# Performance work log

Hardware: AMD Instinct MI355X
Metric: run time of the kernel (lower is better)

## Reference

```python
import jax, jax.numpy as jnp
import numpy as np

D = 64          # slot_size == in_features
S = 8           # num_slots
H = 128         # mlp_hidden_size
N_ITER = 3
EPS = 1e-8


def _ln(x, g, b, eps=1e-5):
    m = jnp.mean(x, axis=-1, keepdims=True)
    v = jnp.var(x, axis=-1, keepdims=True)
    return (x - m) * jax.lax.rsqrt(v + eps) * g + b


def _gru(x, h, w_ih, w_hh, b_ih, b_hh):
    # torch.nn.GRUCell semantics, gate order r, z, n
    gi = x @ w_ih.T + b_ih
    gh = h @ w_hh.T + b_hh
    i_r, i_z, i_n = jnp.split(gi, 3, axis=-1)
    h_r, h_z, h_n = jnp.split(gh, 3, axis=-1)
    r = jax.nn.sigmoid(i_r + h_r)
    z = jax.nn.sigmoid(i_z + h_z)
    n = jnp.tanh(i_n + r * h_n)
    return (1.0 - z) * n + z * h


def setup_inputs() -> dict:
    key = jax.random.key(0)
    ks = jax.random.split(key, 16)
    sc = 0.02
    inp = {
        'inputs': jax.random.normal(ks[0], (64, 16384, D), jnp.float32),
        'slots_init': jax.random.normal(ks[1], (64, S, D), jnp.float32),
        'ln_in_g': jnp.ones((D,), jnp.float32), 'ln_in_b': jnp.zeros((D,), jnp.float32),
        'ln_s_g': jnp.ones((D,), jnp.float32), 'ln_s_b': jnp.zeros((D,), jnp.float32),
        'ln_m_g': jnp.ones((D,), jnp.float32), 'ln_m_b': jnp.zeros((D,), jnp.float32),
        'Wq': jax.random.normal(ks[2], (D, D), jnp.float32) * sc,
        'Wk': jax.random.normal(ks[3], (D, D), jnp.float32) * sc,
        'Wv': jax.random.normal(ks[4], (D, D), jnp.float32) * sc,
        'w_ih': jax.random.normal(ks[5], (3 * D, D), jnp.float32) * sc,
        'w_hh': jax.random.normal(ks[6], (3 * D, D), jnp.float32) * sc,
        'b_ih': jnp.zeros((3 * D,), jnp.float32),
        'b_hh': jnp.zeros((3 * D,), jnp.float32),
        'W1': jax.random.normal(ks[7], (H, D), jnp.float32) * sc,
        'b1': jnp.zeros((H,), jnp.float32),
        'W2': jax.random.normal(ks[8], (D, H), jnp.float32) * sc,
        'b2': jnp.zeros((D,), jnp.float32),
        'slots_mu': jax.random.normal(ks[9], (1, 1, D), jnp.float32) * sc,
        'slots_log_sigma': jax.random.normal(ks[10], (1, 1, D), jnp.float32) * sc,
    }
    return inp


def reference(inputs, slots_init, ln_in_g, ln_in_b, ln_s_g, ln_s_b, ln_m_g, ln_m_b,
              Wq, Wk, Wv, w_ih, w_hh, b_ih, b_hh, W1, b1, W2, b2,
              slots_mu, slots_log_sigma):
    B, N, _ = inputs.shape
    x = _ln(inputs, ln_in_g, ln_in_b)
    k = x @ Wk.T                               # [B, N, D]
    v = x @ Wv.T                               # [B, N, D]
    slots = slots_mu + jnp.exp(slots_log_sigma) * slots_init  # [B, S, D]
    scale = D ** -0.5
    attns = None
    for it in range(N_ITER):
        slots_prev = slots
        sn = _ln(slots, ln_s_g, ln_s_b)
        q = sn @ Wq.T                          # [B, S, D]
        logits = scale * jnp.einsum('bnd,bsd->bns', k, q)  # [B, N, S]
        attn = jax.nn.softmax(logits, axis=-1)
        if it == 0:
            attns = jax.lax.stop_gradient(attn)  # clone().detach() on first iter
        else:
            attns = attns + attn
        a = attn + EPS
        a = a / jnp.sum(a, axis=1, keepdims=True)  # normalize over inputs
        updates = jnp.einsum('bns,bnd->bsd', a, v)  # [B, S, D]
        h = _gru(updates.reshape(B * S, D), slots_prev.reshape(B * S, D),
                 w_ih, w_hh, b_ih, b_hh).reshape(B, S, D)
        mlp_out = jnp.maximum(_ln(h, ln_m_g, ln_m_b) @ W1.T + b1, 0.0) @ W2.T + b2
        slots = h + mlp_out
    return slots, attns / N_ITER
```

## Files before the change

### kernel.cpp

```cpp
#include <hip/hip_runtime.h>
#include <math.h>

#define Dk 64
#define Sk 8
#define Nk 16384
#define Bk 64
#define Hk 128
#define BSD (Bk*Sk*Dk)

typedef __attribute__((ext_vector_type(8))) short   bf16x8;
typedef __attribute__((ext_vector_type(4))) float   f32x4;
typedef __attribute__((ext_vector_type(2))) unsigned int u32x2;
typedef __attribute__((ext_vector_type(4))) unsigned int u32x4;

union FragU { u32x4 u; bf16x8 s; };

__device__ __forceinline__ unsigned short f2b(float f){
  unsigned u = __float_as_uint(f);
  unsigned r = (u + 0x7FFFu + ((u>>16)&1u)) >> 16;
  return (unsigned short)r;
}
__device__ __forceinline__ unsigned pk2(float a, float b){
  return (unsigned)f2b(a) | ((unsigned)f2b(b)<<16);
}
__device__ __forceinline__ bf16x8 mkfrag(unsigned a0,unsigned a1,unsigned a2,unsigned a3){
  FragU x; x.u = (u32x4){a0,a1,a2,a3}; return x.s;
}
__device__ __forceinline__ bf16x8 mkfrag2(u32x2 a, u32x2 b){
  FragU x; x.u = (u32x4){a.x,a.y,b.x,b.y}; return x.s;
}
__device__ __forceinline__ float wsum64(float v){
  #pragma unroll
  for (int m=1;m<64;m<<=1) v += __shfl_xor(v,m,64);
  return v;
}
__device__ __forceinline__ f32x4 ntld4(const float* p){
  return __builtin_nontemporal_load((const f32x4*)p);
}

#define MFMA16(a,b,c) __builtin_amdgcn_mfma_f32_16x16x32_bf16(a,b,c,0,0,0)
#define TRRD(dst, addr)          asm volatile("ds_read_b64_tr_b16 %0, %1"              : "=v"(dst) : "v"(addr) : "memory")
#define TRRD_O(dst, addr, OFF)   asm volatile("ds_read_b64_tr_b16 %0, %1 offset:" #OFF : "=v"(dst) : "v"(addr) : "memory")

template<int MODE, int LAST>
__global__ __launch_bounds__(256,4) void iter_kernel(
    const float* __restrict__ inp, unsigned short* __restrict__ xbf,
    const float* __restrict__ ln_g, const float* __restrict__ ln_b,
    const float* __restrict__ qtb,
    float* __restrict__ attns_out,
    float* __restrict__ Upart,
    float* __restrict__ denpart)
{
  constexpr int NQ = LAST ? 3 : 1;
  __shared__ unsigned short shmem[4*2688];
  __shared__ float ured[4][512];
  __shared__ float dred[4][8];

  const int t   = threadIdx.x;
  const int wid = t>>6, l = t&63;
  const int r16 = l&15, g = l>>4;
  unsigned short* sh = &shmem[wid*2688];
  const unsigned ldsb = (unsigned)(unsigned long long)(void*)sh;

  const int blk = blockIdx.x;
  const int gw  = blk*4 + wid;
  const int b   = gw>>7;
  const int w0  = (gw&127)*4;

  bf16x8 qf0[NQ], qf1[NQ];
  #pragma unroll
  for (int it=0; it<NQ; ++it){
    const float* qp = qtb + (size_t)it*BSD + (size_t)((b<<3) + (r16&7))*Dk + g*8;
    f32x4 a0 = *(const f32x4*)(qp);    f32x4 a1 = *(const f32x4*)(qp+4);
    f32x4 c0 = *(const f32x4*)(qp+32); f32x4 c1 = *(const f32x4*)(qp+36);
    qf0[it] = mkfrag(pk2(a0.x,a0.y),pk2(a0.z,a0.w),pk2(a1.x,a1.y),pk2(a1.z,a1.w));
    qf1[it] = mkfrag(pk2(c0.x,c0.y),pk2(c0.z,c0.w),pk2(c1.x,c1.y),pk2(c1.z,c1.w));
  }

  f32x4 uacc0={0.f,0.f,0.f,0.f}, uacc1={0.f,0.f,0.f,0.f};
  f32x4 uacc2={0.f,0.f,0.f,0.f}, uacc3={0.f,0.f,0.f,0.f};
  f32x4 dacc = {0.f,0.f,0.f,0.f};

  f32x4 gv0,gv1,gv2,gv3, bv0,bv1,bv2,bv3;
  if (MODE==0){
    const float* gp  = ln_g + g*8;      const float* bp  = ln_b + g*8;
    const float* gp2 = ln_g + 32 + g*8; const float* bp2 = ln_b + 32 + g*8;
    gv0=*(const f32x4*)gp;  gv1=*(const f32x4*)(gp+4);
    gv2=*(const f32x4*)gp2; gv3=*(const f32x4*)(gp2+4);
    bv0=*(const f32x4*)bp;  bv1=*(const f32x4*)(bp+4);
    bv2=*(const f32x4*)bp2; bv3=*(const f32x4*)(bp2+4);
  }

  f32x4 nx[2][4];
  u32x4 np[2][2];
  u32x4 fr[2][2];

  auto LOADW = [&](int w){
    const size_t base = (size_t)b*Nk + (size_t)(w0+w)*32;
    #pragma unroll
    for (int rt=0; rt<2; ++rt){
      const size_t row = base + rt*16 + r16;
      if (MODE==0){
        const float* s0 = inp + row*Dk + g*8;
        const float* s1 = inp + row*Dk + 32 + g*8;
        nx[rt][0]=ntld4(s0); nx[rt][1]=ntld4(s0+4);
        nx[rt][2]=ntld4(s1); nx[rt][3]=ntld4(s1+4);
      } else {
        const unsigned short* sp = xbf + row*Dk;
        np[rt][0] = *(const u32x4*)(sp + g*8);
        np[rt][1] = *(const u32x4*)(sp + 32 + g*8);
      }
    }
  };

  auto PROCESS = [&](int w){
    const size_t base = (size_t)b*Nk + (size_t)(w0+w)*32;
    #pragma unroll
    for (int rt=0; rt<2; ++rt){
      const int rloc = rt*16 + r16;
      u32x4 q0, q1;
      if (MODE==0){
        f32x4 x0=nx[rt][0], x1=nx[rt][1], x2=nx[rt][2], x3=nx[rt][3];
        float s1 = (x0.x+x0.y+x0.z+x0.w)+(x1.x+x1.y+x1.z+x1.w)
                 + (x2.x+x2.y+x2.z+x2.w)+(x3.x+x3.y+x3.z+x3.w);
        float s2 = x0.x*x0.x+x0.y*x0.y+x0.z*x0.z+x0.w*x0.w
                 + x1.x*x1.x+x1.y*x1.y+x1.z*x1.z+x1.w*x1.w
                 + x2.x*x2.x+x2.y*x2.y+x2.z*x2.z+x2.w*x2.w
                 + x3.x*x3.x+x3.y*x3.y+x3.z*x3.z+x3.w*x3.w;
        s1 += __shfl_xor(s1,16,64); s1 += __shfl_xor(s1,32,64);
        s2 += __shfl_xor(s2,16,64); s2 += __shfl_xor(s2,32,64);
        const float mean = s1*(1.f/64.f);
        const float rstd = rsqrtf(s2*(1.f/64.f) - mean*mean + 1e-5f);
        x0 = (x0-mean)*rstd*gv0 + bv0;  x1 = (x1-mean)*rstd*gv1 + bv1;
        x2 = (x2-mean)*rstd*gv2 + bv2;  x3 = (x3-mean)*rstd*gv3 + bv3;
        q0 = (u32x4){pk2(x0.x,x0.y),pk2(x0.z,x0.w),pk2(x1.x,x1.y),pk2(x1.z,x1.w)};
        q1 = (u32x4){pk2(x2.x,x2.y),pk2(x2.z,x2.w),pk2(x3.x,x3.y),pk2(x3.z,x3.w)};
        const size_t row = base + rloc;
        *(u32x4*)(xbf + row*Dk + g*8)      = q0;
        *(u32x4*)(xbf + row*Dk + 32 + g*8) = q1;
      } else {
        q0 = np[rt][0]; q1 = np[rt][1];
      }
      fr[rt][0] = q0; fr[rt][1] = q1;
      const int i0 = (g>>1)*528     + rloc*16 + (g&1)*8;
      const int i1 = ((g>>1)+2)*528 + rloc*16 + (g&1)*8;
      *(u32x4*)&sh[i0] = q0;
      *(u32x4*)&sh[i1] = q1;
    }
  };

  LOADW(0); PROCESS(0); LOADW(1);

  for (int w4=0; w4<4; ++w4){
    const size_t rowwin = (size_t)b*Nk + (size_t)(w0+w4)*32;

    #pragma unroll
    for (int rt=0; rt<2; ++rt){
      FragU fl, fh; fl.u = fr[rt][0]; fh.u = fr[rt][1];
      const bf16x8 xl = fl.s, xh = fh.s;
      f32x4 asum = {0.f,0.f,0.f,0.f};
      f32x4 atc;
      #pragma unroll
      for (int it=0; it<NQ; ++it){
        f32x4 c = {0.f,0.f,0.f,0.f};
        c = MFMA16(qf0[it], xl, c);
        c = MFMA16(qf1[it], xh, c);
        float mx = fmaxf(fmaxf(c.x,c.y), fmaxf(c.z,c.w));
        mx = fmaxf(mx, __shfl_xor(mx,16,64));
        f32x4 e;
        e.x = __expf(c.x-mx); e.y = __expf(c.y-mx);
        e.z = __expf(c.z-mx); e.w = __expf(c.w-mx);
        float es = e.x+e.y+e.z+e.w;
        es += __shfl_xor(es,16,64);
        f32x4 at = e*(1.f/es);
        if (LAST) asum = asum + at;
        atc = at;
      }
      if (LAST && l < 32){
        f32x4 nv = asum*(1.f/3.f);
        __builtin_nontemporal_store(nv,
            (f32x4*)(attns_out + (rowwin + rt*16 + r16)*Sk + g*4));
      }
      f32x4 a = atc + 1e-8f;
      dacc = dacc + a;
      u32x2 pk = {pk2(a.x,a.y), pk2(a.z,a.w)};
      *(u32x2*)&sh[2112 + (rt*16+r16)*16 + g*4] = pk;
    }

    u32x2 p0,p1, b00,b01,b10,b11,b20,b21,b30,b31;
    const unsigned xA = ldsb + g*256 + r16*2;
    const unsigned pA = ldsb + 4224 + g*256 + r16*2;
    TRRD  (b00, xA);          TRRD_O(b01, xA, 128);
    TRRD_O(b10, xA, 1056);    TRRD_O(b11, xA, 1184);
    TRRD_O(b20, xA, 2112);    TRRD_O(b21, xA, 2240);
    TRRD_O(b30, xA, 3168);    TRRD_O(b31, xA, 3296);
    TRRD  (p0, pA);           TRRD_O(p1, pA, 128);

    if (w4 < 3) PROCESS(w4+1);
    if (w4 < 2) LOADW(w4+2);

    if (w4 < 3) asm volatile("s_waitcnt lgkmcnt(4)" ::: "memory");
    else        asm volatile("s_waitcnt lgkmcnt(0)" ::: "memory");
    __builtin_amdgcn_sched_barrier(0);

    const bf16x8 pf = mkfrag2(p0,p1);
    uacc0 = MFMA16(pf, mkfrag2(b00,b01), uacc0);
    uacc1 = MFMA16(pf, mkfrag2(b10,b11), uacc1);
    uacc2 = MFMA16(pf, mkfrag2(b20,b21), uacc2);
    uacc3 = MFMA16(pf, mkfrag2(b30,b31), uacc3);
  }

  float dd0=dacc.x, dd1=dacc.y, dd2=dacc.z, dd3=dacc.w;
  #pragma unroll
  for (int m=1;m<16;m<<=1){
    dd0 += __shfl_xor(dd0,m,64); dd1 += __shfl_xor(dd1,m,64);
    dd2 += __shfl_xor(dd2,m,64); dd3 += __shfl_xor(dd3,m,64);
  }
  if (l < 32){
    #pragma unroll
    for (int j=0;j<4;++j){
      ured[wid][(g*4+j)*64 +  0 + r16] = uacc0[j];
      ured[wid][(g*4+j)*64 + 16 + r16] = uacc1[j];
      ured[wid][(g*4+j)*64 + 32 + r16] = uacc2[j];
      ured[wid][(g*4+j)*64 + 48 + r16] = uacc3[j];
    }
    if (r16 == 0){
      dred[wid][g*4+0]=dd0; dred[wid][g*4+1]=dd1;
      dred[wid][g*4+2]=dd2; dred[wid][g*4+3]=dd3;
    }
  }
  __syncthreads();
  #pragma unroll
  for (int e=t; e<512; e+=256){
    Upart[(size_t)blk*512 + e] = ured[0][e]+ured[1][e]+ured[2][e]+ured[3][e];
  }
  if (t < 8) denpart[blk*8 + t] = dred[0][t]+dred[1][t]+dred[2][t]+dred[3][t];
}

__global__ __launch_bounds__(64) void slot_kernel(
    const float* __restrict__ slots_init,
    const float* __restrict__ mu, const float* __restrict__ lsig,
    const float* __restrict__ ln_s_g, const float* __restrict__ ln_s_b,
    const float* __restrict__ ln_m_g, const float* __restrict__ ln_m_b,
    const float* __restrict__ Wq, const float* __restrict__ Wk, const float* __restrict__ Wv,
    const float* __restrict__ w_ih, const float* __restrict__ w_hh,
    const float* __restrict__ b_ih, const float* __restrict__ b_hh,
    const float* __restrict__ W1, const float* __restrict__ b1,
    const float* __restrict__ W2, const float* __restrict__ b2,
    float* __restrict__ slots, const float* __restrict__ Upart,
    const float* __restrict__ denpart,
    float* __restrict__ qt_out, float* __restrict__ slots_out, int mode)
{
  __shared__ float sh[Hk];
  __shared__ float shh[Dk];
  const int d  = threadIdx.x;
  const int bs = blockIdx.x;

  float snew;
  if (mode == 0) {
    snew = mu[d] + expf(lsig[d]) * slots_init[bs*Dk + d];
  } else {
    const int b8 = bs>>3, s = bs&7;
    const float* up = Upart + (size_t)(b8*32)*512 + s*64 + d;
    float uval = 0.f;
    #pragma unroll 8
    for (int k2=0;k2<32;++k2) uval += up[k2*512];
    float dp = (d<32) ? denpart[(b8*32+d)*8 + s] : 0.f;
    const float dn = wsum64(dp);

    sh[d] = uval;
    __syncthreads();
    float num = 0.f;
    #pragma unroll
    for (int j=0;j<Dk;j+=4){
      float4 w = *(const float4*)&Wv[d*Dk+j];
      num += sh[j]*w.x + sh[j+1]*w.y + sh[j+2]*w.z + sh[j+3]*w.w;
    }
    const float upd = num / dn;
    const float h = slots[bs*Dk + d];
    __syncthreads();
    sh[d] = upd; shh[d] = h;
    __syncthreads();

    float gi_r=b_ih[d], gi_z=b_ih[Dk+d], gi_n=b_ih[2*Dk+d];
    float gh_r=b_hh[d], gh_z=b_hh[Dk+d], gh_n=b_hh[2*Dk+d];
    #pragma unroll 4
    for (int j=0;j<Dk;j+=4){
      const float x0=sh[j],  x1=sh[j+1],  x2=sh[j+2],  x3=sh[j+3];
      const float h0=shh[j], h1=shh[j+1], h2=shh[j+2], h3=shh[j+3];
      float4 w;
      w = *(const float4*)&w_ih[d*Dk+j];        gi_r += x0*w.x+x1*w.y+x2*w.z+x3*w.w;
      w = *(const float4*)&w_ih[(Dk+d)*Dk+j];   gi_z += x0*w.x+x1*w.y+x2*w.z+x3*w.w;
      w = *(const float4*)&w_ih[(2*Dk+d)*Dk+j]; gi_n += x0*w.x+x1*w.y+x2*w.z+x3*w.w;
      w = *(const float4*)&w_hh[d*Dk+j];        gh_r += h0*w.x+h1*w.y+h2*w.z+h3*w.w;
      w = *(const float4*)&w_hh[(Dk+d)*Dk+j];   gh_z += h0*w.x+h1*w.y+h2*w.z+h3*w.w;
      w = *(const float4*)&w_hh[(2*Dk+d)*Dk+j]; gh_n += h0*w.x+h1*w.y+h2*w.z+h3*w.w;
    }
    const float rg = 1.f/(1.f+expf(-(gi_r+gh_r)));
    const float zg = 1.f/(1.f+expf(-(gi_z+gh_z)));
    const float ng = tanhf(gi_n + rg*gh_n);
    const float hn = (1.f-zg)*ng + zg*h;

    const float m  = wsum64(hn)*(1.f/64.f);
    const float dv = hn - m;
    const float vr = wsum64(dv*dv)*(1.f/64.f);
    const float mv = dv*rsqrtf(vr+1e-5f)*ln_m_g[d] + ln_m_b[d];
    __syncthreads();
    sh[d] = mv;
    __syncthreads();

    float h1a = b1[d], h2a = b1[Dk+d];
    #pragma unroll 4
    for (int j=0;j<Dk;j+=4){
      const float x0=sh[j], x1=sh[j+1], x2=sh[j+2], x3=sh[j+3];
      float4 w;
      w = *(const float4*)&W1[d*Dk+j];      h1a += x0*w.x+x1*w.y+x2*w.z+x3*w.w;
      w = *(const float4*)&W1[(Dk+d)*Dk+j]; h2a += x0*w.x+x1*w.y+x2*w.z+x3*w.w;
    }
    h1a = fmaxf(h1a, 0.f); h2a = fmaxf(h2a, 0.f);
    __syncthreads();
    sh[d] = h1a; sh[Dk+d] = h2a;
    __syncthreads();
    float o = b2[d];
    #pragma unroll 4
    for (int tt=0;tt<Hk;tt+=4){
      float4 w = *(const float4*)&W2[d*Hk+tt];
      o += sh[tt]*w.x + sh[tt+1]*w.y + sh[tt+2]*w.z + sh[tt+3]*w.w;
    }
    snew = hn + o;
  }

  if (slots_out){ slots_out[bs*Dk + d] = snew; return; }
  slots[bs*Dk + d] = snew;

  const float m2  = wsum64(snew)*(1.f/64.f);
  const float dv2 = snew - m2;
  const float vr2 = wsum64(dv2*dv2)*(1.f/64.f);
  const float sn  = dv2*rsqrtf(vr2+1e-5f)*ln_s_g[d] + ln_s_b[d];
  __syncthreads();
  sh[d] = sn;
  __syncthreads();
  float q = 0.f;
  #pragma unroll
  for (int j=0;j<Dk;j+=4){
    float4 w = *(const float4*)&Wq[d*Dk+j];
    q += sh[j]*w.x + sh[j+1]*w.y + sh[j+2]*w.z + sh[j+3]*w.w;
  }
  __syncthreads();
  sh[d] = q;
  __syncthreads();
  float qt = 0.f;
  for (int dd=0; dd<Dk; ++dd) qt += sh[dd]*Wk[dd*Dk + d];
  qt_out[bs*Dk + d] = qt * 0.125f;
}

extern "C" void kernel_launch(void* const* d_in, const int* in_sizes, int n_in,
                              void* d_out, int out_size, void* d_ws, size_t ws_size,
                              hipStream_t stream)
{
  const float* inp     = (const float*)d_in[0];
  const float* sinit   = (const float*)d_in[1];
  const float* ln_in_g = (const float*)d_in[2];
  const float* ln_in_b = (const float*)d_in[3];
  const float* ln_s_g  = (const float*)d_in[4];
  const float* ln_s_b  = (const float*)d_in[5];
  const float* ln_m_g  = (const float*)d_in[6];
  const float* ln_m_b  = (const float*)d_in[7];
  const float* Wq      = (const float*)d_in[8];
  const float* Wk      = (const float*)d_in[9];
  const float* Wv      = (const float*)d_in[10];
  const float* w_ih    = (const float*)d_in[11];
  const float* w_hh    = (const float*)d_in[12];
  const float* b_ih    = (const float*)d_in[13];
  const float* b_hh    = (const float*)d_in[14];
  const float* W1      = (const float*)d_in[15];
  const float* b1      = (const float*)d_in[16];
  const float* W2      = (const float*)d_in[17];
  const float* b2      = (const float*)d_in[18];
  const float* mu      = (const float*)d_in[19];
  const float* lsig    = (const float*)d_in[20];

  float* out       = (float*)d_out;
  float* out_slots = out;
  float* out_attns = out + BSD;

  char* w = (char*)d_ws;
  float* slots   = (float*)(w);
  float* qtbuf   = (float*)(w + 131072);
  float* Upart   = (float*)(w + 655360);
  float* denpart = (float*)(w + 4849664);
  unsigned short* xbf = (unsigned short*)(w + 4915200);

  float* qt0 = qtbuf;
  float* qt1 = qtbuf + BSD;
  float* qt2 = qtbuf + 2*BSD;
  float* qt3 = qtbuf + 3*BSD;

  slot_kernel<<<Bk*Sk, Dk, 0, stream>>>(sinit, mu, lsig, ln_s_g, ln_s_b, ln_m_g, ln_m_b,
      Wq, Wk, Wv, w_ih, w_hh, b_ih, b_hh, W1, b1, W2, b2,
      slots, Upart, denpart, qt0, nullptr, 0);

  iter_kernel<0,0><<<2048, 256, 0, stream>>>(
      inp, xbf, ln_in_g, ln_in_b, qt0, out_attns, Upart, denpart);
  slot_kernel<<<Bk*Sk, Dk, 0, stream>>>(sinit, mu, lsig, ln_s_g, ln_s_b, ln_m_g, ln_m_b,
      Wq, Wk, Wv, w_ih, w_hh, b_ih, b_hh, W1, b1, W2, b2,
      slots, Upart, denpart, qt1, nullptr, 1);

  iter_kernel<1,0><<<2048, 256, 0, stream>>>(
      inp, xbf, ln_in_g, ln_in_b, qt1, out_attns, Upart, denpart);
  slot_kernel<<<Bk*Sk, Dk, 0, stream>>>(sinit, mu, lsig, ln_s_g, ln_s_b, ln_m_g, ln_m_b,
      Wq, Wk, Wv, w_ih, w_hh, b_ih, b_hh, W1, b1, W2, b2,
      slots, Upart, denpart, qt2, nullptr, 1);

  iter_kernel<1,1><<<2048, 256, 0, stream>>>(
      inp, xbf, ln_in_g, ln_in_b, qtbuf, out_attns, Upart, denpart);
  slot_kernel<<<Bk*Sk, Dk, 0, stream>>>(sinit, mu, lsig, ln_s_g, ln_s_b, ln_m_g, ln_m_b,
      Wq, Wk, Wv, w_ih, w_hh, b_ih, b_hh, W1, b1, W2, b2,
      slots, Upart, denpart, qt3, out_slots, 1);
}
```

Before: 232.1 us.

## Fuse slot GRU/MLP update into iteration kernels and halve grid size

Folds the per-slot GRU, MLP and query projection into the prologue of each attention iteration kernel. Every block recomputes the slot state for its batch redundantly from the previous iteration's partial sums, which removes three small slot_kernel launches and the serial gaps between kernels. The grid drops from 2048 to 1024 blocks, and each wave now processes 8 windows instead of 4, which halves the number of partials. The cost is redundant slot math in every block (16x per batch) and a longer prologue before streaming begins. Partial buffers are double-buffered per iteration to avoid read/write hazards.

```diff
diff --git a/kernel.cpp b/kernel.cpp
--- a/kernel.cpp
+++ b/kernel.cpp
@@ -41,20 +41,125 @@
 #define MFMA16(a,b,c) __builtin_amdgcn_mfma_f32_16x16x32_bf16(a,b,c,0,0,0)
 #define TRRD(dst, addr)          asm volatile("ds_read_b64_tr_b16 %0, %1"              : "=v"(dst) : "v"(addr) : "memory")
 #define TRRD_O(dst, addr, OFF)   asm volatile("ds_read_b64_tr_b16 %0, %1 offset:" #OFF : "=v"(dst) : "v"(addr) : "memory")
-
-template<int MODE, int LAST>
+#define LGKM0 asm volatile("s_waitcnt lgkmcnt(0)" ::: "memory")
+
+__device__ __forceinline__ float gru_mlp_step(
+    int d, float uval, float dn, float h,
+    const float* __restrict__ Wv,
+    const float* __restrict__ w_ih, const float* __restrict__ w_hh,
+    const float* __restrict__ b_ih, const float* __restrict__ b_hh,
+    const float* __restrict__ W1, const float* __restrict__ b1,
+    const float* __restrict__ W2, const float* __restrict__ b2,
+    const float* __restrict__ ln_m_g, const float* __restrict__ ln_m_b,
+    float* scr, float* shh)
+{
+  scr[d] = uval; LGKM0;
+  float num = 0.f;
+  #pragma unroll
+  for (int j=0;j<Dk;j+=4){
+    float4 w = *(const float4*)&Wv[d*Dk+j];
+    num += scr[j]*w.x + scr[j+1]*w.y + scr[j+2]*w.z + scr[j+3]*w.w;
+  }
+  const float upd = num / dn;
+  LGKM0;
+  scr[d] = upd; shh[d] = h; LGKM0;
+
+  float gi_r=b_ih[d], gi_z=b_ih[Dk+d], gi_n=b_ih[2*Dk+d];
+  float gh_r=b_hh[d], gh_z=b_hh[Dk+d], gh_n=b_hh[2*Dk+d];
+  #pragma unroll 4
+  for (int j=0;j<Dk;j+=4){
+    const float x0=scr[j],  x1=scr[j+1],  x2=scr[j+2],  x3=scr[j+3];
+    const float h0=shh[j], h1=shh[j+1], h2=shh[j+2], h3=shh[j+3];
+    float4 w;
+    w = *(const float4*)&w_ih[d*Dk+j];        gi_r += x0*w.x+x1*w.y+x2*w.z+x3*w.w;
+    w = *(const float4*)&w_ih[(Dk+d)*Dk+j];   gi_z += x0*w.x+x1*w.y+x2*w.z+x3*w.w;
+    w = *(const float4*)&w_ih[(2*Dk+d)*Dk+j]; gi_n += x0*w.x+x1*w.y+x2*w.z+x3*w.w;
+    w = *(const float4*)&w_hh[d*Dk+j];        gh_r += h0*w.x+h1*w.y+h2*w.z+h3*w.w;
+    w = *(const float4*)&w_hh[(Dk+d)*Dk+j];   gh_z += h0*w.x+h1*w.y+h2*w.z+h3*w.w;
+    w = *(const float4*)&w_hh[(2*Dk+d)*Dk+j]; gh_n += h0*w.x+h1*w.y+h2*w.z+h3*w.w;
+  }
+  const float rg = 1.f/(1.f+expf(-(gi_r+gh_r)));
+  const float zg = 1.f/(1.f+expf(-(gi_z+gh_z)));
+  const float ng = tanhf(gi_n + rg*gh_n);
+  const float hn = (1.f-zg)*ng + zg*h;
+
+  const float m  = wsum64(hn)*(1.f/64.f);
+  const float dv = hn - m;
+  const float vr = wsum64(dv*dv)*(1.f/64.f);
+  const float mv = dv*rsqrtf(vr+1e-5f)*ln_m_g[d] + ln_m_b[d];
+  LGKM0;
+  scr[d] = mv; LGKM0;
+
+  float h1a = b1[d], h2a = b1[Dk+d];
+  #pragma unroll 4
+  for (int j=0;j<Dk;j+=4){
+    const float x0=scr[j], x1=scr[j+1], x2=scr[j+2], x3=scr[j+3];
+    float4 w;
+    w = *(const float4*)&W1[d*Dk+j];      h1a += x0*w.x+x1*w.y+x2*w.z+x3*w.w;
+    w = *(const float4*)&W1[(Dk+d)*Dk+j]; h2a += x0*w.x+x1*w.y+x2*w.z+x3*w.w;
+  }
+  h1a = fmaxf(h1a, 0.f); h2a = fmaxf(h2a, 0.f);
+  LGKM0;
+  scr[d] = h1a; scr[Dk+d] = h2a; LGKM0;
+  float o = b2[d];
+  #pragma unroll 4
+  for (int tt=0;tt<Hk;tt+=4){
+    float4 w = *(const float4*)&W2[d*Hk+tt];
+    o += scr[tt]*w.x + scr[tt+1]*w.y + scr[tt+2]*w.z + scr[tt+3]*w.w;
+  }
+  return hn + o;
+}
+
+__device__ __forceinline__ float qt_from_slot(
+    int d, float snew, const float* __restrict__ ln_s_g, const float* __restrict__ ln_s_b,
+    const float* __restrict__ Wq, const float* __restrict__ Wk, float* scr)
+{
+  const float m2  = wsum64(snew)*(1.f/64.f);
+  const float dv2 = snew - m2;
+  const float vr2 = wsum64(dv2*dv2)*(1.f/64.f);
+  const float sn  = dv2*rsqrtf(vr2+1e-5f)*ln_s_g[d] + ln_s_b[d];
+  LGKM0;
+  scr[d] = sn; LGKM0;
+  float q = 0.f;
+  #pragma unroll
+  for (int j=0;j<Dk;j+=4){
+    float4 w = *(const float4*)&Wq[d*Dk+j];
+    q += scr[j]*w.x + scr[j+1]*w.y + scr[j+2]*w.z + scr[j+3]*w.w;
+  }
+  LGKM0;
+  scr[d] = q; LGKM0;
+  float qt = 0.f;
+  for (int dd=0; dd<Dk; ++dd) qt += scr[dd]*Wk[dd*Dk + d];
+  return qt * 0.125f;
+}
+
+template<int IT>
 __global__ __launch_bounds__(256,4) void iter_kernel(
     const float* __restrict__ inp, unsigned short* __restrict__ xbf,
     const float* __restrict__ ln_g, const float* __restrict__ ln_b,
-    const float* __restrict__ qtb,
+    const float* __restrict__ sinit, const float* __restrict__ mu, const float* __restrict__ lsig,
+    const float* __restrict__ ln_s_g, const float* __restrict__ ln_s_b,
+    const float* __restrict__ ln_m_g, const float* __restrict__ ln_m_b,
+    const float* __restrict__ Wq, const float* __restrict__ Wk, const float* __restrict__ Wv,
+    const float* __restrict__ w_ih, const float* __restrict__ w_hh,
+    const float* __restrict__ b_ih, const float* __restrict__ b_hh,
+    const float* __restrict__ W1, const float* __restrict__ b1,
+    const float* __restrict__ W2, const float* __restrict__ b2,
+    const float* __restrict__ Upart_prev, const float* __restrict__ denpart_prev,
+    const float* __restrict__ slots_prev, float* __restrict__ slots_out,
+    const float* __restrict__ qt01, float* __restrict__ qt_out,
     float* __restrict__ attns_out,
-    float* __restrict__ Upart,
-    float* __restrict__ denpart)
+    float* __restrict__ Upart, float* __restrict__ denpart)
 {
-  constexpr int NQ = LAST ? 3 : 1;
+  constexpr int MODE = (IT==0) ? 0 : 1;
+  constexpr int LAST = (IT==2) ? 1 : 0;
+  constexpr int NQ   = LAST ? 3 : 1;
+
   __shared__ unsigned short shmem[4*2688];
-  __shared__ float ured[4][512];
+  __shared__ float uredA[4][512];
   __shared__ float dred[4][8];
+  __shared__ float pscrA[4][Hk];
+  __shared__ float pshhA[4][Dk];
 
   const int t   = threadIdx.x;
   const int wid = t>>6, l = t&63;
@@ -63,23 +168,8 @@
   const unsigned ldsb = (unsigned)(unsigned long long)(void*)sh;
 
   const int blk = blockIdx.x;
-  const int gw  = blk*4 + wid;
-  const int b   = gw>>7;
-  const int w0  = (gw&127)*4;
-
-  bf16x8 qf0[NQ], qf1[NQ];
-  #pragma unroll
-  for (int it=0; it<NQ; ++it){
-    const float* qp = qtb + (size_t)it*BSD + (size_t)((b<<3) + (r16&7))*Dk + g*8;
-    f32x4 a0 = *(const f32x4*)(qp);    f32x4 a1 = *(const f32x4*)(qp+4);
-    f32x4 c0 = *(const f32x4*)(qp+32); f32x4 c1 = *(const f32x4*)(qp+36);
-    qf0[it] = mkfrag(pk2(a0.x,a0.y),pk2(a0.z,a0.w),pk2(a1.x,a1.y),pk2(a1.z,a1.w));
-    qf1[it] = mkfrag(pk2(c0.x,c0.y),pk2(c0.z,c0.w),pk2(c1.x,c1.y),pk2(c1.z,c1.w));
-  }
-
-  f32x4 uacc0={0.f,0.f,0.f,0.f}, uacc1={0.f,0.f,0.f,0.f};
-  f32x4 uacc2={0.f,0.f,0.f,0.f}, uacc3={0.f,0.f,0.f,0.f};
-  f32x4 dacc = {0.f,0.f,0.f,0.f};
+  const int b   = blk>>4;
+  const int wib = ((blk&15)<<2) + wid;
 
   f32x4 gv0,gv1,gv2,gv3, bv0,bv1,bv2,bv3;
   if (MODE==0){
@@ -96,7 +186,7 @@
   u32x4 fr[2][2];
 
   auto LOADW = [&](int w){
-    const size_t base = (size_t)b*Nk + (size_t)(w0+w)*32;
+    const size_t base = (size_t)b*Nk + (size_t)(wib*8 + w)*32;
     #pragma unroll
     for (int rt=0; rt<2; ++rt){
       const size_t row = base + rt*16 + r16;
@@ -114,7 +204,7 @@
   };
 
   auto PROCESS = [&](int w){
-    const size_t base = (size_t)b*Nk + (size_t)(w0+w)*32;
+    const size_t base = (size_t)b*Nk + (size_t)(wib*8 + w)*32;
     #pragma unroll
     for (int rt=0; rt<2; ++rt){
       const int rloc = rt*16 + r16;
@@ -149,10 +239,68 @@
     }
   };
 
-  LOADW(0); PROCESS(0); LOADW(1);
-
-  for (int w4=0; w4<4; ++w4){
-    const size_t rowwin = (size_t)b*Nk + (size_t)(w0+w4)*32;
+  LOADW(0);
+
+  {
+    float* scr = &pscrA[wid][0];
+    float* shh = &pshhA[wid][0];
+    float* qts = &uredA[0][0];
+    #pragma unroll
+    for (int si=0; si<2; ++si){
+      const int s  = wid + si*4;
+      const int bs = b*Sk + s;
+      const float s0 = mu[l] + expf(lsig[l]) * sinit[bs*Dk + l];
+      float snew;
+      if (IT==0){
+        snew = s0;
+      } else {
+        const float hprev = (IT==1) ? s0 : slots_prev[bs*Dk + l];
+        const float* up = Upart_prev + (size_t)(b*16)*512 + s*64 + l;
+        float uval = 0.f;
+        #pragma unroll
+        for (int k2=0;k2<16;++k2) uval += up[k2*512];
+        float dnv = 0.f;
+        #pragma unroll
+        for (int k2=0;k2<16;++k2) dnv += denpart_prev[(b*16+k2)*Sk + s];
+        snew = gru_mlp_step(l, uval, dnv, hprev, Wv, w_ih, w_hh, b_ih, b_hh,
+                            W1, b1, W2, b2, ln_m_g, ln_m_b, scr, shh);
+        if ((blk&15)==0) slots_out[bs*Dk + l] = snew;
+      }
+      const float qt = qt_from_slot(l, snew, ln_s_g, ln_s_b, Wq, Wk, scr);
+      qts[(NQ-1)*512 + s*64 + l] = qt;
+      if (IT<2 && (blk&15)==0) qt_out[bs*Dk + l] = qt;
+    }
+    if (IT==2){
+      for (int e=t; e<1024; e+=256){
+        const int j = e>>9, rem = e&511;
+        qts[j*512 + rem] = qt01[(size_t)j*BSD + (size_t)b*512 + rem];
+      }
+    }
+  }
+  __syncthreads();
+
+  bf16x8 qf0[NQ], qf1[NQ];
+  {
+    const float* qts = &uredA[0][0];
+    #pragma unroll
+    for (int it=0; it<NQ; ++it){
+      const float* qp = &qts[it*512 + (r16&7)*64 + g*8];
+      f32x4 a0 = *(const f32x4*)(qp);    f32x4 a1 = *(const f32x4*)(qp+4);
+      f32x4 c0 = *(const f32x4*)(qp+32); f32x4 c1 = *(const f32x4*)(qp+36);
+      qf0[it] = mkfrag(pk2(a0.x,a0.y),pk2(a0.z,a0.w),pk2(a1.x,a1.y),pk2(a1.z,a1.w));
+      qf1[it] = mkfrag(pk2(c0.x,c0.y),pk2(c0.z,c0.w),pk2(c1.x,c1.y),pk2(c1.z,c1.w));
+    }
+  }
+  __syncthreads();
+
+  f32x4 uacc0={0.f,0.f,0.f,0.f}, uacc1={0.f,0.f,0.f,0.f};
+  f32x4 uacc2={0.f,0.f,0.f,0.f}, uacc3={0.f,0.f,0.f,0.f};
+  f32x4 dacc = {0.f,0.f,0.f,0.f};
+
+  PROCESS(0); LOADW(1);
+
+  for (int w4=0; w4<8; ++w4){
+    const size_t rowwin = (size_t)b*Nk + (size_t)(wib*8 + w4)*32;
 
     #pragma unroll
     for (int rt=0; rt<2; ++rt){
@@ -196,10 +344,10 @@
     TRRD_O(b30, xA, 3168);    TRRD_O(b31, xA, 3296);
     TRRD  (p0, pA);           TRRD_O(p1, pA, 128);
 
-    if (w4 < 3) PROCESS(w4+1);
-    if (w4 < 2) LOADW(w4+2);
-
-    if (w4 < 3) asm volatile("s_waitcnt lgkmcnt(4)" ::: "memory");
+    if (w4 < 7) PROCESS(w4+1);
+    if (w4 < 6) LOADW(w4+2);
+
+    if (w4 < 7) asm volatile("s_waitcnt lgkmcnt(4)" ::: "memory");
     else        asm volatile("s_waitcnt lgkmcnt(0)" ::: "memory");
     __builtin_amdgcn_sched_barrier(0);
 
@@ -219,10 +367,10 @@
   if (l < 32){
     #pragma unroll
     for (int j=0;j<4;++j){
-      ured[wid][(g*4+j)*64 +  0 + r16] = uacc0[j];
-      ured[wid][(g*4+j)*64 + 16 + r16] = uacc1[j];
-      ured[wid][(g*4+j)*64 + 32 + r16] = uacc2[j];
-      ured[wid][(g*4+j)*64 + 48 + r16] = uacc3[j];
+      uredA[wid][(g*4+j)*64 +  0 + r16] = uacc0[j];
+      uredA[wid][(g*4+j)*64 + 16 + r16] = uacc1[j];
+      uredA[wid][(g*4+j)*64 + 32 + r16] = uacc2[j];
+      uredA[wid][(g*4+j)*64 + 48 + r16] = uacc3[j];
     }
     if (r16 == 0){
       dred[wid][g*4+0]=dd0; dred[wid][g*4+1]=dd1;
@@ -232,126 +380,38 @@
   __syncthreads();
   #pragma unroll
   for (int e=t; e<512; e+=256){
-    Upart[(size_t)blk*512 + e] = ured[0][e]+ured[1][e]+ured[2][e]+ured[3][e];
+    Upart[(size_t)blk*512 + e] = uredA[0][e]+uredA[1][e]+uredA[2][e]+uredA[3][e];
   }
   if (t < 8) denpart[blk*8 + t] = dred[0][t]+dred[1][t]+dred[2][t]+dred[3][t];
 }
 
-__global__ __launch_bounds__(64) void slot_kernel(
-    const float* __restrict__ slots_init,
-    const float* __restrict__ mu, const float* __restrict__ lsig,
-    const float* __restrict__ ln_s_g, const float* __restrict__ ln_s_b,
-    const float* __restrict__ ln_m_g, const float* __restrict__ ln_m_b,
-    const float* __restrict__ Wq, const float* __restrict__ Wk, const float* __restrict__ Wv,
+__global__ __launch_bounds__(64) void fin_kernel(
+    const float* __restrict__ slots2, const float* __restrict__ Upart,
+    const float* __restrict__ denpart,
+    const float* __restrict__ Wv,
     const float* __restrict__ w_ih, const float* __restrict__ w_hh,
     const float* __restrict__ b_ih, const float* __restrict__ b_hh,
     const float* __restrict__ W1, const float* __restrict__ b1,
     const float* __restrict__ W2, const float* __restrict__ b2,
-    float* __restrict__ slots, const float* __restrict__ Upart,
-    const float* __restrict__ denpart,
-    float* __restrict__ qt_out, float* __restrict__ slots_out, int mode)
+    const float* __restrict__ ln_m_g, const float* __restrict__ ln_m_b,
+    float* __restrict__ out_slots)
 {
-  __shared__ float sh[Hk];
+  __shared__ float scr[Hk];
   __shared__ float shh[Dk];
   const int d  = threadIdx.x;
   const int bs = blockIdx.x;
-
-  float snew;
-  if (mode == 0) {
-    snew = mu[d] + expf(lsig[d]) * slots_init[bs*Dk + d];
-  } else {
-    const int b8 = bs>>3, s = bs&7;
-    const float* up = Upart + (size_t)(b8*32)*512 + s*64 + d;
-    float uval = 0.f;
-    #pragma unroll 8
-    for (int k2=0;k2<32;++k2) uval += up[k2*512];
-    float dp = (d<32) ? denpart[(b8*32+d)*8 + s] : 0.f;
-    const float dn = wsum64(dp);
-
-    sh[d] = uval;
-    __syncthreads();
-    float num = 0.f;
-    #pragma unroll
-    for (int j=0;j<Dk;j+=4){
-      float4 w = *(const float4*)&Wv[d*Dk+j];
-      num += sh[j]*w.x + sh[j+1]*w.y + sh[j+2]*w.z + sh[j+3]*w.w;
-    }
-    const float upd = num / dn;
-    const float h = slots[bs*Dk + d];
-    __syncthreads();
-    sh[d] = upd; shh[d] = h;
-    __syncthreads();
-
-    float gi_r=b_ih[d], gi_z=b_ih[Dk+d], gi_n=b_ih[2*Dk+d];
-    float gh_r=b_hh[d], gh_z=b_hh[Dk+d], gh_n=b_hh[2*Dk+d];
-    #pragma unroll 4
-    for (int j=0;j<Dk;j+=4){
-      const float x0=sh[j],  x1=sh[j+1],  x2=sh[j+2],  x3=sh[j+3];
-      const float h0=shh[j], h1=shh[j+1], h2=shh[j+2], h3=shh[j+3];
-      float4 w;
-      w = *(const float4*)&w_ih[d*Dk+j];        gi_r += x0*w.x+x1*w.y+x2*w.z+x3*w.w;
-      w = *(const float4*)&w_ih[(Dk+d)*Dk+j];   gi_z += x0*w.x+x1*w.y+x2*w.z+x3*w.w;
-      w = *(const float4*)&w_ih[(2*Dk+d)*Dk+j]; gi_n += x0*w.x+x1*w.y+x2*w.z+x3*w.w;
-      w = *(const float4*)&w_hh[d*Dk+j];        gh_r += h0*w.x+h1*w.y+h2*w.z+h3*w.w;
-      w = *(const float4*)&w_hh[(Dk+d)*Dk+j];   gh_z += h0*w.x+h1*w.y+h2*w.z+h3*w.w;
-      w = *(const float4*)&w_hh[(2*Dk+d)*Dk+j]; gh_n += h0*w.x+h1*w.y+h2*w.z+h3*w.w;
-    }
-    const float rg = 1.f/(1.f+expf(-(gi_r+gh_r)));
-    const float zg = 1.f/(1.f+expf(-(gi_z+gh_z)));
-    const float ng = tanhf(gi_n + rg*gh_n);
-    const float hn = (1.f-zg)*ng + zg*h;
-
-    const float m  = wsum64(hn)*(1.f/64.f);
-    const float dv = hn - m;
-    const float vr = wsum64(dv*dv)*(1.f/64.f);
-    const float mv = dv*rsqrtf(vr+1e-5f)*ln_m_g[d] + ln_m_b[d];
-    __syncthreads();
-    sh[d] = mv;
-    __syncthreads();
-
-    float h1a = b1[d], h2a = b1[Dk+d];
-    #pragma unroll 4
-    for (int j=0;j<Dk;j+=4){
-      const float x0=sh[j], x1=sh[j+1], x2=sh[j+2], x3=sh[j+3];
-      float4 w;
-      w = *(const float4*)&W1[d*Dk+j];      h1a += x0*w.x+x1*w.y+x2*w.z+x3*w.w;
-      w = *(const float4*)&W1[(Dk+d)*Dk+j]; h2a += x0*w.x+x1*w.y+x2*w.z+x3*w.w;
-    }
-    h1a = fmaxf(h1a, 0.f); h2a = fmaxf(h2a, 0.f);
-    __syncthreads();
-    sh[d] = h1a; sh[Dk+d] = h2a;
-    __syncthreads();
-    float o = b2[d];
-    #pragma unroll 4
-    for (int tt=0;tt<Hk;tt+=4){
-      float4 w = *(const float4*)&W2[d*Hk+tt];
-      o += sh[tt]*w.x + sh[tt+1]*w.y + sh[tt+2]*w.z + sh[tt+3]*w.w;
-    }
-    snew = hn + o;
-  }
-
-  if (slots_out){ slots_out[bs*Dk + d] = snew; return; }
-  slots[bs*Dk + d] = snew;
-
-  const float m2  = wsum64(snew)*(1.f/64.f);
-  const float dv2 = snew - m2;
-  const float vr2 = wsum64(dv2*dv2)*(1.f/64.f);
-  const float sn  = dv2*rsqrtf(vr2+1e-5f)*ln_s_g[d] + ln_s_b[d];
-  __syncthreads();
-  sh[d] = sn;
-  __syncthreads();
-  float q = 0.f;
-  #pragma unroll
-  for (int j=0;j<Dk;j+=4){
-    float4 w = *(const float4*)&Wq[d*Dk+j];
-    q += sh[j]*w.x + sh[j+1]*w.y + sh[j+2]*w.z + sh[j+3]*w.w;
-  }
-  __syncthreads();
-  sh[d] = q;
-  __syncthreads();
-  float qt = 0.f;
-  for (int dd=0; dd<Dk; ++dd) qt += sh[dd]*Wk[dd*Dk + d];
-  qt_out[bs*Dk + d] = qt * 0.125f;
+  const int b  = bs>>3, s = bs&7;
+
+  const float* up = Upart + (size_t)(b*16)*512 + s*64 + d;
+  float uval = 0.f;
+  #pragma unroll
+  for (int k2=0;k2<16;++k2) uval += up[k2*512];
+  float dnv = 0.f;
+  #pragma unroll
+  for (int k2=0;k2<16;++k2) dnv += denpart[(b*16+k2)*Sk + s];
+  const float h = slots2[bs*Dk + d];
+  out_slots[bs*Dk + d] = gru_mlp_step(d, uval, dnv, h, Wv, w_ih, w_hh,
+      b_ih, b_hh, W1, b1, W2, b2, ln_m_g, ln_m_b, scr, shh);
 }
 
 extern "C" void kernel_launch(void* const* d_in, const int* in_sizes, int n_in,
@@ -385,36 +445,36 @@
   float* out_attns = out + BSD;
 
   char* w = (char*)d_ws;
-  float* slots   = (float*)(w);
-  float* qtbuf   = (float*)(w + 131072);
-  float* Upart   = (float*)(w + 655360);
-  float* denpart = (float*)(w + 4849664);
-  unsigned short* xbf = (unsigned short*)(w + 4915200);
-
-  float* qt0 = qtbuf;
-  float* qt1 = qtbuf + BSD;
-  float* qt2 = qtbuf + 2*BSD;
-  float* qt3 = qtbuf + 3*BSD;
-
-  slot_kernel<<<Bk*Sk, Dk, 0, stream>>>(sinit, mu, lsig, ln_s_g, ln_s_b, ln_m_g, ln_m_b,
+  float* qt0    = (float*)(w);
+  float* qt1    = (float*)(w + 131072);
+  float* slots1 = (float*)(w + 262144);
+  float* slots2 = (float*)(w + 393216);
+  float* Upart0 = (float*)(w + 524288);
+  float* Upart1 = (float*)(w + 2621440);
+  float* Upart2 = (float*)(w + 4718592);
+  float* den0   = (float*)(w + 6815744);
+  float* den1   = (float*)(w + 6848512);
+  float* den2   = (float*)(w + 6881280);
+  unsigned short* xbf = (unsigned short*)(w + 6914048);
+
+  iter_kernel<0><<<1024, 256, 0, stream>>>(inp, xbf, ln_in_g, ln_in_b,
+      sinit, mu, lsig, ln_s_g, ln_s_b, ln_m_g, ln_m_b,
       Wq, Wk, Wv, w_ih, w_hh, b_ih, b_hh, W1, b1, W2, b2,
-      slots, Upart, denpart, qt0, nullptr, 0);
-
-  iter_kernel<0,0><<<2048, 256, 0, stream>>>(
-      inp, xbf, ln_in_g, ln_in_b, qt0, out_attns, Upart, denpart);
-  slot_kernel<<<Bk*Sk, Dk, 0, stream>>>(sinit, mu, lsig, ln_s_g, ln_s_b, ln_m_g, ln_m_b,
+      nullptr, nullptr, nullptr, nullptr, nullptr, qt0,
+      out_attns, Upart0, den0);
+
+  iter_kernel<1><<<1024, 256, 0, stream>>>(inp, xbf, ln_in_g, ln_in_b,
+      sinit, mu, lsig, ln_s_g, ln_s_b, ln_m_g, ln_m_b,
       Wq, Wk, Wv, w_ih, w_hh, b_ih, b_hh, W1, b1, W2, b2,
-      slots, Upart, denpart, qt1, nullptr, 1);
-
-  iter_kernel<1,0><<<2048, 256, 0, stream>>>(
-      inp, xbf, ln_in_g, ln_in_b, qt1, out_attns, Upart, denpart);
-  slot_kernel<<<Bk*Sk, Dk, 0, stream>>>(sinit, mu, lsig, ln_s_g, ln_s_b, ln_m_g, ln_m_b,
+      Upart0, den0, nullptr, slots1, nullptr, qt1,
+      out_attns, Upart1, den1);
+
+  iter_kernel<2><<<1024, 256, 0, stream>>>(inp, xbf, ln_in_g, ln_in_b,
+      sinit, mu, lsig, ln_s_g, ln_s_b, ln_m_g, ln_m_b,
       Wq, Wk, Wv, w_ih, w_hh, b_ih, b_hh, W1, b1, W2, b2,
-      slots, Upart, denpart, qt2, nullptr, 1);
-
-  iter_kernel<1,1><<<2048, 256, 0, stream>>>(
-      inp, xbf, ln_in_g, ln_in_b, qtbuf, out_attns, Upart, denpart);
-  slot_kernel<<<Bk*Sk, Dk, 0, stream>>>(sinit, mu, lsig, ln_s_g, ln_s_b, ln_m_g, ln_m_b,
-      Wq, Wk, Wv, w_ih, w_hh, b_ih, b_hh, W1, b1, W2, b2,
-      slots, Upart, denpart, qt3, out_slots, 1);
-}
+      Upart1, den1, slots1, slots2, qt0, nullptr,
+      out_attns, Upart2, den2);
+
+  fin_kernel<<<512, 64, 0, stream>>>(slots2, Upart2, den2,
+      Wv, w_ih, w_hh, b_ih, b_hh, W1, b1, W2, b2, ln_m_g, ln_m_b, out_slots);
+}
```

New measurement: 761.8 us. 3.28x slower.

## Double per-wave work to 8 windows and deepen bf16 prefetch in middle iteration

Applied to the files above, without the earlier changes.

Each wave now handles 8 windows of 32 rows instead of 4, halving the grid to 1024 blocks and the number of partial U/denominator slices reduced by the slot kernel (32 down to 16 per batch). For the non-last bf16 pass, an extra prefetch buffer loads three windows ahead to hide global latency. This lowers the partial-sum write and reduction traffic and per-wave setup, at the cost of more registers, less parallelism across CUs and a longer serial loop per wave.

```diff
diff --git a/kernel.cpp b/kernel.cpp
--- a/kernel.cpp
+++ b/kernel.cpp
@@ -64,8 +64,8 @@
 
   const int blk = blockIdx.x;
   const int gw  = blk*4 + wid;
-  const int b   = gw>>7;
-  const int w0  = (gw&127)*4;
+  const int b   = gw>>6;
+  const int w0  = (gw&63)*8;
 
   bf16x8 qf0[NQ], qf1[NQ];
   #pragma unroll
@@ -92,24 +92,29 @@
   }
 
   f32x4 nx[2][4];
-  u32x4 np[2][2];
+  u32x4 npA[2][2];
+  u32x4 npB[2][2];
   u32x4 fr[2][2];
 
-  auto LOADW = [&](int w){
+  auto LOADW0 = [&](int w){
     const size_t base = (size_t)b*Nk + (size_t)(w0+w)*32;
     #pragma unroll
     for (int rt=0; rt<2; ++rt){
       const size_t row = base + rt*16 + r16;
-      if (MODE==0){
-        const float* s0 = inp + row*Dk + g*8;
-        const float* s1 = inp + row*Dk + 32 + g*8;
-        nx[rt][0]=ntld4(s0); nx[rt][1]=ntld4(s0+4);
-        nx[rt][2]=ntld4(s1); nx[rt][3]=ntld4(s1+4);
-      } else {
-        const unsigned short* sp = xbf + row*Dk;
-        np[rt][0] = *(const u32x4*)(sp + g*8);
-        np[rt][1] = *(const u32x4*)(sp + 32 + g*8);
-      }
+      const float* s0 = inp + row*Dk + g*8;
+      const float* s1 = inp + row*Dk + 32 + g*8;
+      nx[rt][0]=ntld4(s0); nx[rt][1]=ntld4(s0+4);
+      nx[rt][2]=ntld4(s1); nx[rt][3]=ntld4(s1+4);
+    }
+  };
+  auto LOADW1 = [&](int w, u32x4 (*np)[2]){
+    const size_t base = (size_t)b*Nk + (size_t)(w0+w)*32;
+    #pragma unroll
+    for (int rt=0; rt<2; ++rt){
+      const size_t row = base + rt*16 + r16;
+      const unsigned short* sp = xbf + row*Dk;
+      np[rt][0] = *(const u32x4*)(sp + g*8);
+      np[rt][1] = *(const u32x4*)(sp + 32 + g*8);
     }
   };
 
@@ -139,7 +144,7 @@
         *(u32x4*)(xbf + row*Dk + g*8)      = q0;
         *(u32x4*)(xbf + row*Dk + 32 + g*8) = q1;
       } else {
-        q0 = np[rt][0]; q1 = np[rt][1];
+        q0 = npA[rt][0]; q1 = npA[rt][1];
       }
       fr[rt][0] = q0; fr[rt][1] = q1;
       const int i0 = (g>>1)*528     + rloc*16 + (g&1)*8;
@@ -149,9 +154,11 @@
     }
   };
 
-  LOADW(0); PROCESS(0); LOADW(1);
-
-  for (int w4=0; w4<4; ++w4){
+  if (MODE==0){ LOADW0(0); PROCESS(0); LOADW0(1); }
+  else if (!LAST){ LOADW1(0,npA); PROCESS(0); LOADW1(1,npA); LOADW1(2,npB); }
+  else { LOADW1(0,npA); PROCESS(0); LOADW1(1,npA); }
+
+  for (int w4=0; w4<8; ++w4){
     const size_t rowwin = (size_t)b*Nk + (size_t)(w0+w4)*32;
 
     #pragma unroll
@@ -196,10 +203,20 @@
     TRRD_O(b30, xA, 3168);    TRRD_O(b31, xA, 3296);
     TRRD  (p0, pA);           TRRD_O(p1, pA, 128);
 
-    if (w4 < 3) PROCESS(w4+1);
-    if (w4 < 2) LOADW(w4+2);
-
-    if (w4 < 3) asm volatile("s_waitcnt lgkmcnt(4)" ::: "memory");
+    if (w4 < 7) PROCESS(w4+1);
+    if (MODE==0){
+      if (w4 < 6) LOADW0(w4+2);
+    } else if (!LAST){
+      if (w4 < 6){
+        #pragma unroll
+        for (int rt=0; rt<2; ++rt){ npA[rt][0]=npB[rt][0]; npA[rt][1]=npB[rt][1]; }
+      }
+      if (w4 < 5) LOADW1(w4+3, npB);
+    } else {
+      if (w4 < 6) LOADW1(w4+2, npA);
+    }
+
+    if (w4 < 7) asm volatile("s_waitcnt lgkmcnt(4)" ::: "memory");
     else        asm volatile("s_waitcnt lgkmcnt(0)" ::: "memory");
     __builtin_amdgcn_sched_barrier(0);
 
@@ -261,11 +278,11 @@
     snew = mu[d] + expf(lsig[d]) * slots_init[bs*Dk + d];
   } else {
     const int b8 = bs>>3, s = bs&7;
-    const float* up = Upart + (size_t)(b8*32)*512 + s*64 + d;
+    const float* up = Upart + (size_t)(b8*16)*512 + s*64 + d;
     float uval = 0.f;
-    #pragma unroll 8
-    for (int k2=0;k2<32;++k2) uval += up[k2*512];
-    float dp = (d<32) ? denpart[(b8*32+d)*8 + s] : 0.f;
+    #pragma unroll
+    for (int k2=0;k2<16;++k2) uval += up[(size_t)k2*512];
+    float dp = (d<16) ? denpart[(b8*16 + d)*Sk + s] : 0.f;
     const float dn = wsum64(dp);
 
     sh[d] = uval;
@@ -388,8 +405,8 @@
   float* slots   = (float*)(w);
   float* qtbuf   = (float*)(w + 131072);
   float* Upart   = (float*)(w + 655360);
-  float* denpart = (float*)(w + 4849664);
-  unsigned short* xbf = (unsigned short*)(w + 4915200);
+  float* denpart = (float*)(w + 2752512);
+  unsigned short* xbf = (unsigned short*)(w + 2785280);
 
   float* qt0 = qtbuf;
   float* qt1 = qtbuf + BSD;
@@ -400,19 +417,19 @@
       Wq, Wk, Wv, w_ih, w_hh, b_ih, b_hh, W1, b1, W2, b2,
       slots, Upart, denpart, qt0, nullptr, 0);
 
-  iter_kernel<0,0><<<2048, 256, 0, stream>>>(
+  iter_kernel<0,0><<<1024, 256, 0, stream>>>(
       inp, xbf, ln_in_g, ln_in_b, qt0, out_attns, Upart, denpart);
   slot_kernel<<<Bk*Sk, Dk, 0, stream>>>(sinit, mu, lsig, ln_s_g, ln_s_b, ln_m_g, ln_m_b,
       Wq, Wk, Wv, w_ih, w_hh, b_ih, b_hh, W1, b1, W2, b2,
       slots, Upart, denpart, qt1, nullptr, 1);
 
-  iter_kernel<1,0><<<2048, 256, 0, stream>>>(
+  iter_kernel<1,0><<<1024, 256, 0, stream>>>(
       inp, xbf, ln_in_g, ln_in_b, qt1, out_attns, Upart, denpart);
   slot_kernel<<<Bk*Sk, Dk, 0, stream>>>(sinit, mu, lsig, ln_s_g, ln_s_b, ln_m_g, ln_m_b,
       Wq, Wk, Wv, w_ih, w_hh, b_ih, b_hh, W1, b1, W2, b2,
       slots, Upart, denpart, qt2, nullptr, 1);
 
-  iter_kernel<1,1><<<2048, 256, 0, stream>>>(
+  iter_kernel<1,1><<<1024, 256, 0, stream>>>(
       inp, xbf, ln_in_g, ln_in_b, qtbuf, out_attns, Upart, denpart);
   slot_kernel<<<Bk*Sk, Dk, 0, stream>>>(sinit, mu, lsig, ln_s_g, ln_s_b, ln_m_g, ln_m_b,
       Wq, Wk, Wv, w_ih, w_hh, b_ih, b_hh, W1, b1, W2, b2,
```

After: 233.1 us. Within noise of the previous version (+0.4%).
